# Kernel optimization log

Hardware: AMD Instinct MI355X
Metric: run time of the kernel (lower is better)

Reference implementation:

```python
import jax, jax.numpy as jnp
import numpy as np

D_MODEL = 1024
N_HEADS = 16
HEAD_DIM = D_MODEL // N_HEADS
BATCH = 2
SEQ = 2048
MASK_FILL = -10000.0


def setup_inputs() -> dict:
    key = jax.random.key(0)
    ks = jax.random.split(key, 5)
    scale = 1.0 / np.sqrt(D_MODEL)
    return {
        "x": jax.random.normal(ks[0], (BATCH, SEQ, D_MODEL), dtype=jnp.float32),
        "w_q": jax.random.normal(ks[1], (D_MODEL, D_MODEL), dtype=jnp.float32) * scale,
        "w_k": jax.random.normal(ks[2], (D_MODEL, D_MODEL), dtype=jnp.float32) * scale,
        "w_v": jax.random.normal(ks[3], (D_MODEL, D_MODEL), dtype=jnp.float32) * scale,
        "w_o": jax.random.normal(ks[4], (D_MODEL, D_MODEL), dtype=jnp.float32) * scale,
    }


def reference(x, w_q, w_k, w_v, w_o):
    B, S, C = x.shape
    # Linear(bias=False): y = x @ W^T (torch stores W as [out, in])
    q = jnp.einsum("bsc,dc->bsd", x, w_q).reshape(B, S, N_HEADS, HEAD_DIM)
    k = jnp.einsum("bsc,dc->bsd", x, w_k).reshape(B, S, N_HEADS, HEAD_DIM)
    v = jnp.einsum("bsc,dc->bsd", x, w_v).reshape(B, S, N_HEADS, HEAD_DIM)
    # scores: [B, H, S, S]
    scores = jnp.einsum("bqhd,bkhd->bhqk", q, k) / np.sqrt(HEAD_DIM)
    causal = jnp.tril(jnp.ones((S, S), dtype=bool))
    scores = jnp.where(causal, scores, MASK_FILL)
    weights = jax.nn.softmax(scores, axis=-1)
    out = jnp.einsum("bhqk,bkhd->bqhd", weights, v).reshape(B, S, C)
    return jnp.einsum("bsc,dc->bsd", out, w_o)
```

## Files before the change

kernel.cpp:

```cpp
#include <hip/hip_runtime.h>

typedef __attribute__((ext_vector_type(8))) short bf16x8;
typedef __attribute__((ext_vector_type(4))) float floatx4;

static constexpr int SEQ    = 2048;
static constexpr int CDIM   = 1024;
static constexpr int NH     = 16;
static constexpr int HD     = 64;
static constexpr int NBATCH = 2;
static constexpr int MROWS  = NBATCH * SEQ;

static __device__ __forceinline__ short f2bf(float f) {
    union { float f; unsigned u; } x; x.f = f;
    unsigned r = x.u + 0x7fffu + ((x.u >> 16) & 1u);
    return (short)(r >> 16);
}

static __device__ __forceinline__ unsigned pack2bf(float lo, float hi) {
    return ((unsigned)(unsigned short)f2bf(hi) << 16) | (unsigned)(unsigned short)f2bf(lo);
}

static __device__ __forceinline__ unsigned pk2(float lo, float hi) {
    union { float f; unsigned u; } a, b; a.f = lo; b.f = hi;
    return __builtin_amdgcn_perm(b.u + 0x8000u, a.u + 0x8000u, 0x07060302u);
}

static __device__ __forceinline__ float bf2f(short s) {
    union { unsigned u; float f; } x;
    x.u = ((unsigned)(unsigned short)s) << 16;
    return x.f;
}

static __device__ __forceinline__ floatx4 mfma16(bf16x8 a, bf16x8 b, floatx4 c) {
    return __builtin_amdgcn_mfma_f32_16x16x32_bf16(a, b, c, 0, 0, 0);
}

static __device__ __forceinline__ void gl_lds16(const short* g, short* l) {
    __builtin_amdgcn_global_load_lds(
        (const __attribute__((address_space(1))) void*)g,
        (__attribute__((address_space(3))) void*)l, 16, 0, 0);
}

__global__ void convert_all(
    const void* __restrict__ x,  const void* __restrict__ wq,
    const void* __restrict__ wk, const void* __restrict__ wv,
    const void* __restrict__ wo,
    short* __restrict__ xc,  short* __restrict__ wqc, short* __restrict__ wkc,
    short* __restrict__ wvc, short* __restrict__ woc,
    int* __restrict__ flag)
{
    const int tid = threadIdx.x;
    const unsigned short* xs = (const unsigned short*)x;
    int pl = 0;
    for (int i = tid; i < 2048; i += 256) {
        const int e = (xs[2 * i] >> 7) & 0xFF;
        if (e >= 110 && e <= 144) pl++;
    }
    #pragma unroll
    for (int off = 32; off > 0; off >>= 1) pl += __shfl_down(pl, off, 64);
    __shared__ int cnt;
    if (tid == 0) cnt = 0;
    __syncthreads();
    if ((tid & 63) == 0) atomicAdd(&cnt, pl);
    __syncthreads();
    const int f = (cnt < 1024) ? 1 : 0;
    if (blockIdx.x == 0 && blockIdx.y == 0 && tid == 0) *flag = f;

    const int y = blockIdx.y;
    const void* src = (y == 0) ? x  : (y == 1) ? wq : (y == 2) ? wk : (y == 3) ? wv : wo;
    short*      dst = (y == 0) ? xc : (y == 1) ? wqc : (y == 2) ? wkc : (y == 3) ? wvc : woc;
    const int n4 = (y == 0) ? (MROWS * CDIM / 4) : (CDIM * CDIM / 4);

    const int stride = gridDim.x * blockDim.x;
    for (int i = blockIdx.x * blockDim.x + tid; i < n4; i += stride) {
        if (f) {
            const float4 v = ((const float4*)src)[i];
            ((uint2*)dst)[i] = make_uint2(pack2bf(v.x, v.y), pack2bf(v.z, v.w));
        } else {
            ((uint2*)dst)[i] = ((const uint2*)src)[i];
        }
    }
}

__global__ __launch_bounds__(256) void gemm_bt128(
    const short* __restrict__ A,
    const short* __restrict__ W0, const short* __restrict__ W1, const short* __restrict__ W2,
    void* __restrict__ C0, void* __restrict__ C1, void* __restrict__ C2,
    short* __restrict__ VT, const int* __restrict__ flag)
{
    const int m0  = blockIdx.x * 128;
    const int sel = blockIdx.y >> 3;
    const int n0  = (blockIdx.y & 7) * 128;
    const short* W = (sel == 0) ? W0 : ((sel == 1) ? W1 : W2);
    void*        C = (sel == 0) ? C0 : ((sel == 1) ? C1 : C2);
    const bool f32out = (flag != nullptr) && (*flag != 0);
    const bool vtout  = (sel == 2) && (VT != nullptr);

    __shared__ __align__(16) short ta[128 * 64];
    __shared__ __align__(16) short tb[128 * 64];

    const int tid  = threadIdx.x;
    const int lane = tid & 63;
    const int wave = tid >> 6;
    const int quad = lane >> 4;
    const int l16  = lane & 15;
    const int wm   = (wave >> 1) * 64;
    const int wn   = (wave & 1) * 64;

    floatx4 acc[4][4];
    #pragma unroll
    for (int i = 0; i < 4; i++)
        #pragma unroll
        for (int j = 0; j < 4; j++)
            acc[i][j] = 0.0f;

    const int sr8 = lane >> 3;
    const int ug  = ((lane & 7) ^ sr8) * 8;
    const short* Ab = A + (size_t)(m0 + 32 * wave + sr8) * CDIM + ug;
    const short* Wb = W + (size_t)(n0 + 32 * wave + sr8) * CDIM + ug;
    short* ta0 = ta + (32 * wave) * 64;
    short* tb0 = tb + (32 * wave) * 64;

    for (int k0 = 0; k0 < CDIM; k0 += 64) {
        __syncthreads();
        gl_lds16(Ab + k0,             ta0);
        gl_lds16(Ab +  8 * CDIM + k0, ta0 +  8 * 64);
        gl_lds16(Ab + 16 * CDIM + k0, ta0 + 16 * 64);
        gl_lds16(Ab + 24 * CDIM + k0, ta0 + 24 * 64);
        gl_lds16(Wb + k0,             tb0);
        gl_lds16(Wb +  8 * CDIM + k0, tb0 +  8 * 64);
        gl_lds16(Wb + 16 * CDIM + k0, tb0 + 16 * 64);
        gl_lds16(Wb + 24 * CDIM + k0, tb0 + 24 * 64);
        __syncthreads();

        #pragma unroll
        for (int kc = 0; kc < 2; kc++) {
            const int pu = (((kc * 4 + quad) ^ (l16 & 7))) * 8;
            bf16x8 af[4], bw[4];
            #pragma unroll
            for (int i = 0; i < 4; i++)
                af[i] = *(const bf16x8*)(ta + (wm + i * 16 + l16) * 64 + pu);
            #pragma unroll
            for (int j = 0; j < 4; j++)
                bw[j] = *(const bf16x8*)(tb + (wn + j * 16 + l16) * 64 + pu);
            #pragma unroll
            for (int i = 0; i < 4; i++)
                #pragma unroll
                for (int j = 0; j < 4; j++)
                    acc[i][j] = mfma16(af[i], bw[j], acc[i][j]);
        }
    }

    #pragma unroll
    for (int i = 0; i < 4; i++) {
        #pragma unroll
        for (int j = 0; j < 4; j++) {
            const int row0 = m0 + wm + i * 16 + quad * 4;
            const int col  = n0 + wn + j * 16 + l16;
            if (vtout) {
                const int bb  = row0 >> 11;
                const int key = row0 & 2047;
                const size_t idx = ((size_t)(bb * 1024 + col)) * 2048 + key;
                *(uint2*)(VT + idx) = make_uint2(pk2(acc[i][j][0], acc[i][j][1]),
                                                 pk2(acc[i][j][2], acc[i][j][3]));
            } else if (f32out) {
                float* cp = (float*)C + (size_t)row0 * CDIM + col;
                #pragma unroll
                for (int r = 0; r < 4; r++)
                    cp[(size_t)r * CDIM] = acc[i][j][r];
            } else {
                short* cp = (short*)C + (size_t)row0 * CDIM + col;
                #pragma unroll
                for (int r = 0; r < 4; r++)
                    cp[(size_t)r * CDIM] = f2bf(acc[i][j][r]);
            }
        }
    }
}

__global__ __launch_bounds__(256) void gemm_n64(
    const short* __restrict__ A, const short* __restrict__ W,
    void* __restrict__ C, const int* __restrict__ flag)
{
    const int m0 = blockIdx.x * 128;
    const int n0 = blockIdx.y * 64;
    const bool f32out = (flag != nullptr) && (*flag != 0);

    __shared__ __align__(16) short ta[128 * 64];
    __shared__ __align__(16) short tb[64 * 64];

    const int tid  = threadIdx.x;
    const int lane = tid & 63;
    const int wave = tid >> 6;
    const int quad = lane >> 4;
    const int l16  = lane & 15;
    const int wm   = (wave >> 1) * 64;
    const int wn   = (wave & 1) * 32;

    floatx4 acc[4][2];
    #pragma unroll
    for (int i = 0; i < 4; i++)
        #pragma unroll
        for (int j = 0; j < 2; j++)
            acc[i][j] = 0.0f;

    const int sr8 = lane >> 3;
    const int ug  = ((lane & 7) ^ sr8) * 8;
    const short* Ab = A + (size_t)(m0 + 32 * wave + sr8) * CDIM + ug;
    const short* Wb = W + (size_t)(n0 + 16 * wave + sr8) * CDIM + ug;
    short* ta0 = ta + (32 * wave) * 64;
    short* tb0 = tb + (16 * wave) * 64;

    for (int k0 = 0; k0 < CDIM; k0 += 64) {
        __syncthreads();
        gl_lds16(Ab + k0,             ta0);
        gl_lds16(Ab +  8 * CDIM + k0, ta0 +  8 * 64);
        gl_lds16(Ab + 16 * CDIM + k0, ta0 + 16 * 64);
        gl_lds16(Ab + 24 * CDIM + k0, ta0 + 24 * 64);
        gl_lds16(Wb + k0,             tb0);
        gl_lds16(Wb +  8 * CDIM + k0, tb0 +  8 * 64);
        __syncthreads();

        #pragma unroll
        for (int kc = 0; kc < 2; kc++) {
            const int pu = (((kc * 4 + quad) ^ (l16 & 7))) * 8;
            bf16x8 af[4], bw[2];
            #pragma unroll
            for (int i = 0; i < 4; i++)
                af[i] = *(const bf16x8*)(ta + (wm + i * 16 + l16) * 64 + pu);
            #pragma unroll
            for (int j = 0; j < 2; j++)
                bw[j] = *(const bf16x8*)(tb + (wn + j * 16 + l16) * 64 + pu);
            #pragma unroll
            for (int i = 0; i < 4; i++)
                #pragma unroll
                for (int j = 0; j < 2; j++)
                    acc[i][j] = mfma16(af[i], bw[j], acc[i][j]);
        }
    }

    #pragma unroll
    for (int i = 0; i < 4; i++) {
        #pragma unroll
        for (int j = 0; j < 2; j++) {
            const int row0 = m0 + wm + i * 16 + quad * 4;
            const int col  = n0 + wn + j * 16 + l16;
            if (f32out) {
                float* cp = (float*)C + (size_t)row0 * CDIM + col;
                #pragma unroll
                for (int r = 0; r < 4; r++)
                    cp[(size_t)r * CDIM] = acc[i][j][r];
            } else {
                short* cp = (short*)C + (size_t)row0 * CDIM + col;
                #pragma unroll
                for (int r = 0; r < 4; r++)
                    cp[(size_t)r * CDIM] = f2bf(acc[i][j][r]);
            }
        }
    }
}

__global__ __launch_bounds__(256, 2) void attn_t(
    const short* __restrict__ Q, const short* __restrict__ K,
    const short* __restrict__ VT,
    short* __restrict__ P0, short* __restrict__ P1, float* __restrict__ L)
{
    const int h = blockIdx.x;
    const int b = blockIdx.y;
    const int z = blockIdx.z;
    const int g = z >> 3;
    const int item = (g == 1) ? (23 - z) : (g == 3) ? (55 - z) : z;
    const int qt2 = 15 - (item >> 1);
    const int p   = item & 1;
    const int nktall = qt2 + 1;

    const int tid  = threadIdx.x;
    const int lane = tid & 63;
    const int wave = tid >> 6;
    const int quad = lane >> 4;
    const int l16  = lane & 15;

    __shared__ __align__(16) short Kt[128][72];
    __shared__ __align__(16) short Vt[64][136];
    __shared__ __align__(16) short Pl[4][2][16][136];

    const int rowBase = b * SEQ;
    const int colH    = h * HD;
    const int qgA     = qt2 * 128 + wave * 16 + l16;
    const int qgB     = qgA + 64;

    bf16x8 qa0, qa1, qc0, qc1;
    {
        const short* qp = Q + (size_t)(rowBase + qgA) * CDIM + colH + quad * 8;
        qa0 = *(const bf16x8*)qp;
        qa1 = *(const bf16x8*)(qp + 32);
        const short* qp2 = qp + (size_t)64 * CDIM;
        qc0 = *(const bf16x8*)qp2;
        qc1 = *(const bf16x8*)(qp2 + 32);
    }

    floatx4 oA[4], oB[4];
    #pragma unroll
    for (int nd = 0; nd < 4; nd++) { oA[nd] = 0.0f; oB[nd] = 0.0f; }
    float lA = 0.0f, lB = 0.0f;

    const int kk = tid >> 1;
    const int kd = (tid & 1) * 32;
    const short* kg = K + (size_t)(rowBase + kk) * CDIM + colH + kd;
    const int sd = tid >> 2;
    const int sk = (tid & 3) * 32;
    const short* vg = VT + ((size_t)(b * NH + h) * HD + sd) * SEQ + sk;

    const short* kg0 = kg + (size_t)p * 128 * CDIM;
    const short* vg0 = vg + p * 128;
    uint4 ka_0 = *(const uint4*)(kg0);
    uint4 ka_1 = *(const uint4*)(kg0 + 8);
    uint4 ka_2 = *(const uint4*)(kg0 + 16);
    uint4 ka_3 = *(const uint4*)(kg0 + 24);
    uint4 va_0 = *(const uint4*)(vg0);
    uint4 va_1 = *(const uint4*)(vg0 + 8);
    uint4 va_2 = *(const uint4*)(vg0 + 16);
    uint4 va_3 = *(const uint4*)(vg0 + 24);

    for (int kt = p; kt < nktall; kt += 2) {
        __syncthreads();
        *(uint4*)&Kt[kk][kd]      = ka_0;
        *(uint4*)&Kt[kk][kd + 8]  = ka_1;
        *(uint4*)&Kt[kk][kd + 16] = ka_2;
        *(uint4*)&Kt[kk][kd + 24] = ka_3;
        *(uint4*)&Vt[sd][sk]      = va_0;
        *(uint4*)&Vt[sd][sk + 8]  = va_1;
        *(uint4*)&Vt[sd][sk + 16] = va_2;
        *(uint4*)&Vt[sd][sk + 24] = va_3;
        __syncthreads();

        if (kt + 2 < nktall) {
            const short* kn = kg + (size_t)(kt + 2) * 128 * CDIM;
            const short* vn = vg + (kt + 2) * 128;
            ka_0 = *(const uint4*)(kn);
            ka_1 = *(const uint4*)(kn + 8);
            ka_2 = *(const uint4*)(kn + 16);
            ka_3 = *(const uint4*)(kn + 24);
            va_0 = *(const uint4*)(vn);
            va_1 = *(const uint4*)(vn + 8);
            va_2 = *(const uint4*)(vn + 16);
            va_3 = *(const uint4*)(vn + 24);
        }

        const int key0 = kt * 128;
        const bool masked = (kt == nktall - 1);

        #pragma unroll
        for (int ms = 0; ms < 8; ms++) {
            const short* kp = &Kt[ms * 16 + l16][quad * 8];
            bf16x8 k0 = *(const bf16x8*)kp;
            bf16x8 k1 = *(const bf16x8*)(kp + 32);
            floatx4 sA = {0.f, 0.f, 0.f, 0.f};
            floatx4 sB = {0.f, 0.f, 0.f, 0.f};
            sA = mfma16(k0, qa0, sA);
            sB = mfma16(k0, qc0, sB);
            sA = mfma16(k1, qa1, sA);
            sB = mfma16(k1, qc1, sB);
            float pA[4], pB[4];
            #pragma unroll
            for (int r = 0; r < 4; r++) {
                const int kgl = key0 + ms * 16 + quad * 4 + r;
                float eA = __expf(sA[r] * 0.125f);
                float eB = __expf(sB[r] * 0.125f);
                if (masked) {
                    if (kgl > qgA) eA = 0.0f;
                    if (kgl > qgB) eB = 0.0f;
                }
                pA[r] = eA; lA += eA;
                pB[r] = eB; lB += eB;
            }
            *(uint2*)&Pl[wave][0][l16][ms * 16 + quad * 4] =
                make_uint2(pk2(pA[0], pA[1]), pk2(pA[2], pA[3]));
            *(uint2*)&Pl[wave][1][l16][ms * 16 + quad * 4] =
                make_uint2(pk2(pB[0], pB[1]), pk2(pB[2], pB[3]));
        }

        #pragma unroll
        for (int kc = 0; kc < 4; kc++) {
            const bf16x8 pbA = *(const bf16x8*)&Pl[wave][0][l16][kc * 32 + quad * 8];
            const bf16x8 pbB = *(const bf16x8*)&Pl[wave][1][l16][kc * 32 + quad * 8];
            #pragma unroll
            for (int nd = 0; nd < 4; nd++) {
                const bf16x8 va = *(const bf16x8*)&Vt[nd * 16 + l16][kc * 32 + quad * 8];
                oA[nd] = mfma16(va, pbA, oA[nd]);
                oB[nd] = mfma16(va, pbB, oB[nd]);
            }
        }
    }

    lA += __shfl_xor(lA, 16, 64);
    lA += __shfl_xor(lA, 32, 64);
    lB += __shfl_xor(lB, 16, 64);
    lB += __shfl_xor(lB, 32, 64);

    short* Pp = p ? P1 : P0;
    float* Lp = L + p * (NBATCH * NH * SEQ);
    short* opA = Pp + (size_t)(rowBase + qgA) * CDIM + colH;
    short* opB = Pp + (size_t)(rowBase + qgB) * CDIM + colH;
    #pragma unroll
    for (int nd = 0; nd < 4; nd++) {
        *(uint2*)(opA + nd * 16 + quad * 4) =
            make_uint2(pk2(oA[nd][0], oA[nd][1]), pk2(oA[nd][2], oA[nd][3]));
        *(uint2*)(opB + nd * 16 + quad * 4) =
            make_uint2(pk2(oB[nd][0], oB[nd][1]), pk2(oB[nd][2], oB[nd][3]));
    }
    if (quad == 0) {
        Lp[(b * NH + h) * SEQ + qgA] = lA;
        Lp[(b * NH + h) * SEQ + qgB] = lB;
    }
}

__global__ void combine(const short* __restrict__ P0, const short* __restrict__ P1,
                        const float* __restrict__ L, short* __restrict__ Ob)
{
    const int i = blockIdx.x * blockDim.x + threadIdx.x;
    const int row = i >> 7;
    const int c8  = i & 127;
    const int h   = c8 >> 3;
    const int b   = row >> 11;
    const int q   = row & 2047;
    const int li  = (b * NH + h) * SEQ + q;
    const float inv = 1.0f / (L[li] + L[NBATCH * NH * SEQ + li]);

    const bf16x8 a0 = ((const bf16x8*)P0)[i];
    const bf16x8 a1 = ((const bf16x8*)P1)[i];
    unsigned d[4];
    #pragma unroll
    for (int e = 0; e < 4; e++) {
        const float lo = (bf2f(a0[2 * e])     + bf2f(a1[2 * e]))     * inv;
        const float hi = (bf2f(a0[2 * e + 1]) + bf2f(a1[2 * e + 1])) * inv;
        d[e] = pk2(lo, hi);
    }
    ((uint4*)Ob)[i] = make_uint4(d[0], d[1], d[2], d[3]);
}

extern "C" void kernel_launch(void* const* d_in, const int* in_sizes, int n_in,
                              void* d_out, int out_size, void* d_ws, size_t ws_size,
                              hipStream_t stream)
{
    const void* x  = d_in[0];
    const void* wq = d_in[1];
    const void* wk = d_in[2];
    const void* wv = d_in[3];
    const void* wo = d_in[4];

    int* flag = (int*)d_ws;
    short* w = (short*)((char*)d_ws + 256);
    const int ME  = 1024 * 1024;
    short* Wqc = w;
    short* Wkc = w + 1 * ME;
    short* Wvc = w + 2 * ME;
    short* Woc = w + 3 * ME;
    short* Xc  = w + 4 * ME;
    short* Qb  = w + 8 * ME;
    short* Kb  = w + 12 * ME;
    short* VTb = w + 16 * ME;
    short* P1b = w + 20 * ME;
    float* Lb  = (float*)(w + 24 * ME);
    short* P0b = Xc;
    short* Ob  = Xc;

    dim3 blk(256);
    convert_all<<<dim3(512, 5), blk, 0, stream>>>(
        x, wq, wk, wv, wo, Xc, Wqc, Wkc, Wvc, Woc, flag);

    gemm_bt128<<<dim3(MROWS / 128, 24), blk, 0, stream>>>(
        Xc, Wqc, Wkc, Wvc, Qb, Kb, nullptr, VTb, nullptr);
    attn_t<<<dim3(NH, NBATCH, 32), blk, 0, stream>>>(Qb, Kb, VTb, P0b, P1b, Lb);
    combine<<<dim3(MROWS * CDIM / 8 / 256), blk, 0, stream>>>(P0b, P1b, Lb, Ob);
    gemm_n64<<<dim3(MROWS / 128, CDIM / 64), blk, 0, stream>>>(
        Ob, Woc, d_out, flag);
}
```

Measured before the change: 175.1 us.

## Keep softmax P in registers by permuting V layout, drop LDS P buffer

```diff
diff --git a/kernel.cpp b/kernel.cpp
--- a/kernel.cpp
+++ b/kernel.cpp
@@ -33,6 +33,12 @@
 
 static __device__ __forceinline__ floatx4 mfma16(bf16x8 a, bf16x8 b, floatx4 c) {
     return __builtin_amdgcn_mfma_f32_16x16x32_bf16(a, b, c, 0, 0, 0);
+}
+
+static __device__ __forceinline__ bf16x8 mk8(unsigned d0, unsigned d1, unsigned d2, unsigned d3) {
+    union { unsigned u[4]; bf16x8 v; } x;
+    x.u[0] = d0; x.u[1] = d1; x.u[2] = d2; x.u[3] = d3;
+    return x.v;
 }
 
 static __device__ __forceinline__ void gl_lds16(const short* g, short* l) {
@@ -260,7 +266,7 @@
     }
 }
 
-__global__ __launch_bounds__(256, 2) void attn_t(
+__global__ __launch_bounds__(256, 4) void attn_t(
     const short* __restrict__ Q, const short* __restrict__ K,
     const short* __restrict__ VT,
     short* __restrict__ P0, short* __restrict__ P1, float* __restrict__ L)
@@ -282,7 +288,6 @@
 
     __shared__ __align__(16) short Kt[128][72];
     __shared__ __align__(16) short Vt[64][136];
-    __shared__ __align__(16) short Pl[4][2][16][136];
 
     const int rowBase = b * SEQ;
     const int colH    = h * HD;
@@ -322,16 +327,25 @@
     uint4 va_2 = *(const uint4*)(vg0 + 16);
     uint4 va_3 = *(const uint4*)(vg0 + 24);
 
+    const float SCL = 0.18033688011112042f;
+
     for (int kt = p; kt < nktall; kt += 2) {
         __syncthreads();
         *(uint4*)&Kt[kk][kd]      = ka_0;
         *(uint4*)&Kt[kk][kd + 8]  = ka_1;
         *(uint4*)&Kt[kk][kd + 16] = ka_2;
         *(uint4*)&Kt[kk][kd + 24] = ka_3;
-        *(uint4*)&Vt[sd][sk]      = va_0;
-        *(uint4*)&Vt[sd][sk + 8]  = va_1;
-        *(uint4*)&Vt[sd][sk + 16] = va_2;
-        *(uint4*)&Vt[sd][sk + 24] = va_3;
+        {
+            short* vrow = &Vt[sd][sk];
+            *(uint2*)(vrow + 0)  = make_uint2(va_0.x, va_0.y);
+            *(uint2*)(vrow + 8)  = make_uint2(va_0.z, va_0.w);
+            *(uint2*)(vrow + 16) = make_uint2(va_1.x, va_1.y);
+            *(uint2*)(vrow + 24) = make_uint2(va_1.z, va_1.w);
+            *(uint2*)(vrow + 4)  = make_uint2(va_2.x, va_2.y);
+            *(uint2*)(vrow + 12) = make_uint2(va_2.z, va_2.w);
+            *(uint2*)(vrow + 20) = make_uint2(va_3.x, va_3.y);
+            *(uint2*)(vrow + 28) = make_uint2(va_3.z, va_3.w);
+        }
         __syncthreads();
 
         if (kt + 2 < nktall) {
@@ -350,6 +364,7 @@
         const int key0 = kt * 128;
         const bool masked = (kt == nktall - 1);
 
+        unsigned hA0 = 0, hA1 = 0, hB0 = 0, hB1 = 0;
         #pragma unroll
         for (int ms = 0; ms < 8; ms++) {
             const short* kp = &Kt[ms * 16 + l16][quad * 8];
@@ -365,8 +380,8 @@
             #pragma unroll
             for (int r = 0; r < 4; r++) {
                 const int kgl = key0 + ms * 16 + quad * 4 + r;
-                float eA = __expf(sA[r] * 0.125f);
-                float eB = __expf(sB[r] * 0.125f);
+                float eA = exp2f(sA[r] * SCL);
+                float eB = exp2f(sB[r] * SCL);
                 if (masked) {
                     if (kgl > qgA) eA = 0.0f;
                     if (kgl > qgB) eB = 0.0f;
@@ -374,21 +389,22 @@
                 pA[r] = eA; lA += eA;
                 pB[r] = eB; lB += eB;
             }
-            *(uint2*)&Pl[wave][0][l16][ms * 16 + quad * 4] =
-                make_uint2(pk2(pA[0], pA[1]), pk2(pA[2], pA[3]));
-            *(uint2*)&Pl[wave][1][l16][ms * 16 + quad * 4] =
-                make_uint2(pk2(pB[0], pB[1]), pk2(pB[2], pB[3]));
-        }
-
-        #pragma unroll
-        for (int kc = 0; kc < 4; kc++) {
-            const bf16x8 pbA = *(const bf16x8*)&Pl[wave][0][l16][kc * 32 + quad * 8];
-            const bf16x8 pbB = *(const bf16x8*)&Pl[wave][1][l16][kc * 32 + quad * 8];
-            #pragma unroll
-            for (int nd = 0; nd < 4; nd++) {
-                const bf16x8 va = *(const bf16x8*)&Vt[nd * 16 + l16][kc * 32 + quad * 8];
-                oA[nd] = mfma16(va, pbA, oA[nd]);
-                oB[nd] = mfma16(va, pbB, oB[nd]);
+            const unsigned cA0 = pk2(pA[0], pA[1]);
+            const unsigned cA1 = pk2(pA[2], pA[3]);
+            const unsigned cB0 = pk2(pB[0], pB[1]);
+            const unsigned cB1 = pk2(pB[2], pB[3]);
+            if ((ms & 1) == 0) {
+                hA0 = cA0; hA1 = cA1; hB0 = cB0; hB1 = cB1;
+            } else {
+                const int kc = ms >> 1;
+                const bf16x8 pbA = mk8(hA0, hA1, cA0, cA1);
+                const bf16x8 pbB = mk8(hB0, hB1, cB0, cB1);
+                #pragma unroll
+                for (int nd = 0; nd < 4; nd++) {
+                    const bf16x8 va = *(const bf16x8*)&Vt[nd * 16 + l16][kc * 32 + quad * 8];
+                    oA[nd] = mfma16(va, pbA, oA[nd]);
+                    oB[nd] = mfma16(va, pbB, oB[nd]);
+                }
             }
         }
     }
```

Measured after the change: 174.7 us. No clear change (-0.3%).
